# Optimization experiments

Measured on AMD Instinct MI355X. Metric: run time of the kernel, lower is better.

The kernel has to match this reference:

```python
import jax, jax.numpy as jnp
import numpy as np

N, E, F_IN, F_E, HID, HEADS = 20000, 320000, 256, 32, 128, 4
NEG_SLOPE = 0.2  # PyG GATConv default negative_slope


def _segment_softmax(logits, seg, num_segments):
    # logits: [E, H] softmax over edges sharing the same destination node
    m = jax.ops.segment_max(logits, seg, num_segments=num_segments)
    m = jnp.where(jnp.isfinite(m), m, 0.0)
    e = jnp.exp(logits - m[seg])
    s = jax.ops.segment_sum(e, seg, num_segments=num_segments)
    return e / s[seg]


def _gat_layer(x, edge_attr, src, dst, W, We, a_src, a_dst, a_edge, bias, num_nodes):
    H, C = a_src.shape
    h = (x @ W).reshape(-1, H, C)            # [N, H, C]
    he = (edge_attr @ We).reshape(-1, H, C)  # [E, H, C]
    alpha = (h * a_src).sum(-1)[src] + (h * a_dst).sum(-1)[dst] + (he * a_edge).sum(-1)
    alpha = jax.nn.leaky_relu(alpha, NEG_SLOPE)          # [E, H]
    alpha = _segment_softmax(alpha, dst, num_nodes)
    out = jax.ops.segment_sum(h[src] * alpha[..., None], dst, num_segments=num_nodes)
    return out.reshape(num_nodes, H * C) + bias


def setup_inputs() -> dict:
    key = jax.random.key(0)
    ks = jax.random.split(key, 20)
    s1 = 1.0 / np.sqrt(F_IN)
    s2 = 1.0 / np.sqrt(HID * HEADS)
    se = 1.0 / np.sqrt(F_E)
    sh = 1.0 / np.sqrt(HID)
    return {
        "x": jax.random.normal(ks[0], (N, F_IN), jnp.float32),
        "edge_index": jax.random.randint(ks[1], (2, E), 0, N),
        "edge_attr": jax.random.normal(ks[2], (E, F_E), jnp.float32),
        # GAT layer 1: in=F_IN, heads=HEADS, out=HID, concat=True
        "W1": jax.random.normal(ks[3], (F_IN, HEADS * HID), jnp.float32) * s1,
        "We1": jax.random.normal(ks[4], (F_E, HEADS * HID), jnp.float32) * se,
        "as1": jax.random.normal(ks[5], (HEADS, HID), jnp.float32) * sh,
        "ad1": jax.random.normal(ks[6], (HEADS, HID), jnp.float32) * sh,
        "ae1": jax.random.normal(ks[7], (HEADS, HID), jnp.float32) * sh,
        "b1": jnp.zeros((HEADS * HID,), jnp.float32),
        # GAT layer 2: in=HEADS*HID, heads=1, out=HID
        "W2": jax.random.normal(ks[8], (HEADS * HID, HID), jnp.float32) * s2,
        "We2": jax.random.normal(ks[9], (F_E, HID), jnp.float32) * se,
        "as2": jax.random.normal(ks[10], (1, HID), jnp.float32) * sh,
        "ad2": jax.random.normal(ks[11], (1, HID), jnp.float32) * sh,
        "ae2": jax.random.normal(ks[12], (1, HID), jnp.float32) * sh,
        "b2": jnp.zeros((HID,), jnp.float32),
        # projection head: Linear(HID,HID) -> PReLU -> Linear(HID,HID)
        "P1": jax.random.normal(ks[13], (HID, HID), jnp.float32) * sh,
        "pb1": jnp.zeros((HID,), jnp.float32),
        "prelu_a": jnp.float32(0.25),
        "P2": jax.random.normal(ks[14], (HID, HID), jnp.float32) * sh,
        "pb2": jnp.zeros((HID,), jnp.float32),
    }


def reference(x, edge_index, edge_attr, W1, We1, as1, ad1, ae1, b1,
              W2, We2, as2, ad2, ae2, b2, P1, pb1, prelu_a, P2, pb2):
    # eval mode: edge dropout / feature dropout are no-ops
    ei = jnp.concatenate([edge_index, edge_index[::-1]], axis=1)  # add reversed edges
    ea = jnp.concatenate([edge_attr, edge_attr], axis=0)
    src, dst = ei[0], ei[1]
    n = x.shape[0]
    h = jax.nn.elu(_gat_layer(x, ea, src, dst, W1, We1, as1, ad1, ae1, b1, n))
    h = jax.nn.elu(_gat_layer(h, ea, src, dst, W2, We2, as2, ad2, ae2, b2, n))
    z = h @ P1 + pb1
    z = jnp.where(z > 0, z, prelu_a * z)  # PReLU (single shared parameter)
    h_proj = z @ P2 + pb2
    g = jax.nn.sigmoid(h_proj.mean(axis=0))
    return h_proj, g
```

## Files before the change

kernel.cpp:

```cpp
#include <hip/hip_runtime.h>
#include <hip/hip_bf16.h>


#define NN    20000
#define EE    320000
#define E2    640000
#define FIN   256
#define FE    32
#define HIDD  128
#define NHEAD 4
#define HH    512

typedef unsigned short ushort_t;
typedef short frag8 __attribute__((ext_vector_type(8)));
typedef float f32x4 __attribute__((ext_vector_type(4)));

__device__ inline ushort_t f2bf(float f){
  unsigned x = __float_as_uint(f);
  unsigned r = (x + 0x7fffu + ((x>>16)&1u)) >> 16;
  return (ushort_t)r;
}
__device__ inline float bf2f(ushort_t u){ return __uint_as_float(((unsigned)u)<<16); }
__device__ inline float lo_of(unsigned v){ return __uint_as_float(v<<16); }
__device__ inline float hi_of(unsigned v){ return __uint_as_float(v & 0xffff0000u); }

__global__ void prep(const int* __restrict__ ei, int* __restrict__ cnt,
                     const float* __restrict__ x, ushort_t* __restrict__ xb,
                     const float* __restrict__ W1, ushort_t* __restrict__ W1t,
                     const float* __restrict__ W2, ushort_t* __restrict__ W2t,
                     const float* __restrict__ P1, ushort_t* __restrict__ P1th, ushort_t* __restrict__ P1tl,
                     const float* __restrict__ P2, ushort_t* __restrict__ P2th, ushort_t* __restrict__ P2tl,
                     const float* __restrict__ We1, const float* __restrict__ ae1,
                     const float* __restrict__ We2, const float* __restrict__ ae2,
                     float* __restrict__ v1, float* __restrict__ v2){
  int b = blockIdx.x, tid = threadIdx.x;
  if(b < 2500){
    int e = b*256 + tid;
    int dst = (e < EE) ? ei[EE + e] : ei[e - EE];
    atomicAdd(&cnt[dst], 1);
  } else if(b < 7500){
    int i = (b-2500)*256 + tid;
    float4 v = ((const float4*)x)[i];
    ushort4 o; o.x=f2bf(v.x); o.y=f2bf(v.y); o.z=f2bf(v.z); o.w=f2bf(v.w);
    ((ushort4*)xb)[i] = o;
  } else if(b < 8012){
    int idx = (b-7500)*256 + tid;
    int k = idx>>9, n = idx&511;
    W1t[n*FIN + k] = f2bf(W1[idx]);
  } else if(b < 8268){
    int idx = (b-8012)*256 + tid;
    int k = idx>>7, n = idx&127;
    W2t[n*HH + k] = f2bf(W2[idx]);
  } else if(b < 8332){
    int idx = (b-8268)*256 + tid;
    int k = idx>>7, n = idx&127;
    float v = P1[idx];
    ushort_t h = f2bf(v);
    P1th[n*HIDD + k] = h;
    P1tl[n*HIDD + k] = f2bf(v - bf2f(h));
  } else if(b < 8396){
    int idx = (b-8332)*256 + tid;
    int k = idx>>7, n = idx&127;
    float v = P2[idx];
    ushort_t h = f2bf(v);
    P2th[n*HIDD + k] = h;
    P2tl[n*HIDD + k] = f2bf(v - bf2f(h));
  } else {
    if(tid < FE*NHEAD){
      int f = tid>>2, h = tid&3;
      float s = 0.f;
      for(int c=0;c<HIDD;c++) s += We1[f*HH + h*HIDD + c] * ae1[h*HIDD + c];
      v1[f*4+h] = s;
    } else if(tid < FE*NHEAD + FE){
      int f = tid - FE*NHEAD;
      float s = 0.f;
      for(int c=0;c<HIDD;c++) s += We2[f*HIDD + c] * ae2[c];
      v2[f] = s;
    }
  }
}

__global__ void scan_k(const int* __restrict__ cnt, int* __restrict__ rowptr){
  __shared__ int sums[1024];
  int tid = threadIdx.x;
  const int per = (NN + 1023)/1024;
  int base = tid*per;
  int s = 0;
  for(int i=0;i<per;i++){ int idx=base+i; if(idx<NN) s += cnt[idx]; }
  sums[tid] = s; __syncthreads();
  for(int off=1; off<1024; off<<=1){
    int v = (tid>=off)? sums[tid-off] : 0;
    __syncthreads();
    sums[tid] += v;
    __syncthreads();
  }
  int run = (tid==0)? 0 : sums[tid-1];
  for(int i=0;i<per;i++){
    int idx = base+i;
    if(idx<=NN) rowptr[idx] = run;
    if(idx<NN)  run += cnt[idx];
  }
}

__global__ void csr_fill(const int* __restrict__ ei, const float* __restrict__ ea,
                         const float* __restrict__ v1, const float* __restrict__ v2,
                         const int* __restrict__ rowptr, int* __restrict__ fcnt,
                         int* __restrict__ csrc, float* __restrict__ cae1, float* __restrict__ cae2){
  __shared__ float sv1[FE*NHEAD];
  __shared__ float sv2[FE];
  int tid = threadIdx.x;
  if(tid < FE*NHEAD) sv1[tid] = v1[tid];
  if(tid < FE)       sv2[tid] = v2[tid];
  __syncthreads();
  int e = blockIdx.x*256 + tid;
  int a = ei[e], b = ei[EE+e];
  const float4* er4 = (const float4*)(ea + (long)e*FE);
  float a0=0,a1=0,a2=0,a3=0,ab=0;
  #pragma unroll
  for(int f4=0; f4<FE/4; f4++){
    float4 t = er4[f4];
    float tv[4] = {t.x, t.y, t.z, t.w};
    #pragma unroll
    for(int c=0;c<4;c++){
      int f = f4*4+c;
      float t1 = tv[c];
      a0 += t1*sv1[f*4+0]; a1 += t1*sv1[f*4+1]; a2 += t1*sv1[f*4+2]; a3 += t1*sv1[f*4+3];
      ab += t1*sv2[f];
    }
  }
  int pos = rowptr[b] + atomicAdd(&fcnt[b], 1);
  csrc[pos] = a;
  cae1[pos*4+0]=a0; cae1[pos*4+1]=a1; cae1[pos*4+2]=a2; cae1[pos*4+3]=a3;
  cae2[pos] = ab;
  pos = rowptr[a] + atomicAdd(&fcnt[a], 1);
  csrc[pos] = b;
  cae1[pos*4+0]=a0; cae1[pos*4+1]=a1; cae1[pos*4+2]=a2; cae1[pos*4+3]=a3;
  cae2[pos] = ab;
}

__global__ __launch_bounds__(256) void mfma_gemm(const ushort_t* __restrict__ A, const ushort_t* __restrict__ Bt,
                                                 ushort_t* __restrict__ C, int M, int N, int K){
  __shared__ ushort_t As[128*32];
  __shared__ ushort_t Bs[128*32];
  int tid = threadIdx.x;
  int m0 = blockIdx.y*128, n0 = blockIdx.x*128;
  int w = tid>>6, lane = tid&63;
  int qr = (w>>1)*64, qc = (w&1)*64;
  int lrow = lane&15, koff = (lane>>4)*8;
  f32x4 acc[4][4] = {};
  for(int k0=0; k0<K; k0+=32){
    #pragma unroll
    for(int rep=0;rep<2;rep++){
      int segid = tid + rep*256;
      int row = segid>>2, off = (segid&3)*8;
      int gr = m0 + row;
      int4 va = (gr<M) ? *(const int4*)(A + (long)gr*K + k0 + off) : int4{0,0,0,0};
      *(int4*)&As[row*32 + off] = va;
      int4 vb = *(const int4*)(Bt + (long)(n0+row)*K + k0 + off);
      *(int4*)&Bs[row*32 + off] = vb;
    }
    __syncthreads();
    frag8 af[4], bfr[4];
    #pragma unroll
    for(int i=0;i<4;i++) af[i]  = *(const frag8*)&As[(qr + i*16 + lrow)*32 + koff];
    #pragma unroll
    for(int j=0;j<4;j++) bfr[j] = *(const frag8*)&Bs[(qc + j*16 + lrow)*32 + koff];
    #pragma unroll
    for(int i=0;i<4;i++)
      #pragma unroll
      for(int j=0;j<4;j++)
        acc[i][j] = __builtin_amdgcn_mfma_f32_16x16x32_bf16(af[i], bfr[j], acc[i][j], 0,0,0);
    __syncthreads();
  }
  #pragma unroll
  for(int i=0;i<4;i++)
    #pragma unroll
    for(int j=0;j<4;j++)
      #pragma unroll
      for(int r=0;r<4;r++){
        int row = m0 + qr + i*16 + (lane>>4)*4 + r;
        int col = n0 + qc + j*16 + (lane&15);
        if(row<M) C[(long)row*N + col] = f2bf(acc[i][j][r]);
      }
}

__global__ __launch_bounds__(256) void mfma_gemm64(const ushort_t* __restrict__ A, const ushort_t* __restrict__ Bt,
                                                   ushort_t* __restrict__ C, int M, int N, int K){
  __shared__ ushort_t As[64*32];
  __shared__ ushort_t Bs[128*32];
  int tid = threadIdx.x;
  int m0 = blockIdx.y*64, n0 = blockIdx.x*128;
  int w = tid>>6, lane = tid&63;
  int qc = w*32;
  int lrow = lane&15, koff = (lane>>4)*8;
  f32x4 acc[4][2] = {};
  for(int k0=0; k0<K; k0+=32){
    {
      int row = tid>>2, off = (tid&3)*8;
      int gr = m0 + row;
      int4 va = (gr<M) ? *(const int4*)(A + (long)gr*K + k0 + off) : int4{0,0,0,0};
      *(int4*)&As[row*32 + off] = va;
    }
    #pragma unroll
    for(int rep=0;rep<2;rep++){
      int segid = tid + rep*256;
      int row = segid>>2, off = (segid&3)*8;
      int4 vb = *(const int4*)(Bt + (long)(n0+row)*K + k0 + off);
      *(int4*)&Bs[row*32 + off] = vb;
    }
    __syncthreads();
    frag8 af[4], bfr[2];
    #pragma unroll
    for(int i=0;i<4;i++) af[i]  = *(const frag8*)&As[(i*16 + lrow)*32 + koff];
    #pragma unroll
    for(int j=0;j<2;j++) bfr[j] = *(const frag8*)&Bs[(qc + j*16 + lrow)*32 + koff];
    #pragma unroll
    for(int i=0;i<4;i++)
      #pragma unroll
      for(int j=0;j<2;j++)
        acc[i][j] = __builtin_amdgcn_mfma_f32_16x16x32_bf16(af[i], bfr[j], acc[i][j], 0,0,0);
    __syncthreads();
  }
  #pragma unroll
  for(int i=0;i<4;i++)
    #pragma unroll
    for(int j=0;j<2;j++)
      #pragma unroll
      for(int r=0;r<4;r++){
        int row = m0 + i*16 + (lane>>4)*4 + r;
        int col = n0 + qc + j*16 + (lane&15);
        if(row<M) C[(long)row*N + col] = f2bf(acc[i][j][r]);
      }
}

__global__ __launch_bounds__(256) void mfma_proj(const float* __restrict__ A,
                                                 const ushort_t* __restrict__ Bth, const ushort_t* __restrict__ Btl,
                                                 float* __restrict__ C, int M,
                                                 const float* __restrict__ bias,
                                                 const float* __restrict__ prelu_a, int epi){
  __shared__ ushort_t Ash[64*32], Asl[64*32];
  __shared__ ushort_t Bsh[128*32], Bsl[128*32];
  int tid = threadIdx.x;
  int m0 = blockIdx.x*64;
  int w = tid>>6, lane = tid&63;
  int qc = w*32;
  int lrow = lane&15, koff2 = (lane>>4)*8;
  f32x4 acc[4][2] = {};
  for(int k0=0; k0<128; k0+=32){
    {
      int row = tid>>2, koff = (tid&3)*8;
      int gr = m0 + row;
      float4 u0{0,0,0,0}, u1{0,0,0,0};
      if(gr<M){
        u0 = *(const float4*)(A + (long)gr*HIDD + k0 + koff);
        u1 = *(const float4*)(A + (long)gr*HIDD + k0 + koff + 4);
      }
      float vv[8] = {u0.x,u0.y,u0.z,u0.w,u1.x,u1.y,u1.z,u1.w};
      unsigned ph[4], pl[4];
      #pragma unroll
      for(int c=0;c<4;c++){
        ushort_t h0 = f2bf(vv[2*c]),   l0 = f2bf(vv[2*c]   - bf2f(h0));
        ushort_t h1 = f2bf(vv[2*c+1]), l1 = f2bf(vv[2*c+1] - bf2f(h1));
        ph[c] = (unsigned)h0 | ((unsigned)h1<<16);
        pl[c] = (unsigned)l0 | ((unsigned)l1<<16);
      }
      *(uint4*)&Ash[row*32 + koff] = *(uint4*)ph;
      *(uint4*)&Asl[row*32 + koff] = *(uint4*)pl;
    }
    #pragma unroll
    for(int rep=0;rep<2;rep++){
      int segid = tid + rep*256;
      int row = segid>>2, off = (segid&3)*8;
      *(int4*)&Bsh[row*32 + off] = *(const int4*)(Bth + (long)row*HIDD + k0 + off);
      *(int4*)&Bsl[row*32 + off] = *(const int4*)(Btl + (long)row*HIDD + k0 + off);
    }
    __syncthreads();
    frag8 afh[4], afl[4], bfh[2], bfl[2];
    #pragma unroll
    for(int i=0;i<4;i++){
      afh[i] = *(const frag8*)&Ash[(i*16 + lrow)*32 + koff2];
      afl[i] = *(const frag8*)&Asl[(i*16 + lrow)*32 + koff2];
    }
    #pragma unroll
    for(int j=0;j<2;j++){
      bfh[j] = *(const frag8*)&Bsh[(qc + j*16 + lrow)*32 + koff2];
      bfl[j] = *(const frag8*)&Bsl[(qc + j*16 + lrow)*32 + koff2];
    }
    #pragma unroll
    for(int i=0;i<4;i++)
      #pragma unroll
      for(int j=0;j<2;j++){
        acc[i][j] = __builtin_amdgcn_mfma_f32_16x16x32_bf16(afh[i], bfh[j], acc[i][j], 0,0,0);
        acc[i][j] = __builtin_amdgcn_mfma_f32_16x16x32_bf16(afh[i], bfl[j], acc[i][j], 0,0,0);
        acc[i][j] = __builtin_amdgcn_mfma_f32_16x16x32_bf16(afl[i], bfh[j], acc[i][j], 0,0,0);
      }
    __syncthreads();
  }
  float ap = (epi==1)? prelu_a[0] : 0.f;
  #pragma unroll
  for(int i=0;i<4;i++)
    #pragma unroll
    for(int j=0;j<2;j++)
      #pragma unroll
      for(int r=0;r<4;r++){
        int row = m0 + i*16 + (lane>>4)*4 + r;
        int col = qc + j*16 + (lane&15);
        if(row<M){
          float v = acc[i][j][r] + bias[col];
          if(epi==1) v = v>0.f? v : ap*v;
          C[(long)row*HIDD + col] = v;
        }
      }
}


__global__ void node_attn1(const ushort_t* __restrict__ h1b, const float* __restrict__ as1,
                           const float* __restrict__ ad1, float* __restrict__ s1n, float* __restrict__ d1n){
  int n = blockIdx.x;
  int wv = threadIdx.x>>6, lane = threadIdx.x&63;
  unsigned v = *(const unsigned*)(h1b + (long)n*HH + wv*HIDD + 2*lane);
  float f0 = lo_of(v), f1 = hi_of(v);
  float s = f0*as1[wv*HIDD+2*lane] + f1*as1[wv*HIDD+2*lane+1];
  float d = f0*ad1[wv*HIDD+2*lane] + f1*ad1[wv*HIDD+2*lane+1];
  #pragma unroll
  for(int o=32;o>0;o>>=1){ s += __shfl_xor(s,o,64); d += __shfl_xor(d,o,64); }
  if(lane==0){ s1n[n*4+wv]=s; d1n[n*4+wv]=d; }
}

__global__ void node_attn2(const ushort_t* __restrict__ h2b, const float* __restrict__ as2,
                           const float* __restrict__ ad2, float* __restrict__ s2n, float* __restrict__ d2n){
  int n = blockIdx.x*4 + (threadIdx.x>>6);
  int lane = threadIdx.x&63;
  unsigned v = *(const unsigned*)(h2b + (long)n*HIDD + 2*lane);
  float f0 = lo_of(v), f1 = hi_of(v);
  float s = f0*as2[2*lane] + f1*as2[2*lane+1];
  float d = f0*ad2[2*lane] + f1*ad2[2*lane+1];
  #pragma unroll
  for(int o=32;o>0;o>>=1){ s += __shfl_xor(s,o,64); d += __shfl_xor(d,o,64); }
  if(lane==0){ s2n[n]=s; d2n[n]=d; }
}


__global__ void agg1(const ushort_t* __restrict__ h1b, const int* __restrict__ rowptr,
                     const int* __restrict__ csrc,
                     const float* __restrict__ s1n, const float* __restrict__ d1n,
                     const float* __restrict__ cae1, float* __restrict__ elog,
                     const float* __restrict__ b1, ushort_t* __restrict__ out1b){
  int n = blockIdx.x*4 + (threadIdx.x>>6);
  int lane = threadIdx.x&63;
  int beg = rowptr[n], end = rowptr[n+1];
  int h12 = lane&3;
  float dh = d1n[n*4 + h12];
  float m = -1e30f, ss = 0.f;
  for(int base=beg; base<end; base+=16){
    int e = base + (lane>>2);
    if(e<end){
      float t = s1n[csrc[e]*4 + h12] + dh + cae1[e*4 + h12];
      t = t>0.f? t : 0.2f*t;
      elog[e*4 + h12] = t;
      float nm = fmaxf(m, t);
      ss = ss*__expf(m-nm) + __expf(t-nm);
      m = nm;
    }
  }
  #pragma unroll
  for(int o=4;o<=32;o<<=1){
    float mo = __shfl_xor(m, o, 64), so = __shfl_xor(ss, o, 64);
    float nm = fmaxf(m, mo);
    ss = ss*__expf(m-nm) + so*__expf(mo-nm);
    m = nm;
  }
  float inv = ss>0.f ? 1.f/ss : 0.f;
  int hq = lane>>4;
  float mq   = __shfl(m,   hq, 64);
  float invq = __shfl(inv, hq, 64);
  float acc[8] = {};
  int i = beg;
  for(; i+3<end; i+=4){
    int s0 = csrc[i], s1 = csrc[i+1], s2 = csrc[i+2], s3 = csrc[i+3];
    float w0 = __expf(elog[i*4 + hq]     - mq)*invq;
    float w1 = __expf(elog[(i+1)*4 + hq] - mq)*invq;
    float w2 = __expf(elog[(i+2)*4 + hq] - mq)*invq;
    float w3 = __expf(elog[(i+3)*4 + hq] - mq)*invq;
    uint4 v0 = *(const uint4*)(h1b + (long)s0*HH + lane*8);
    uint4 v1 = *(const uint4*)(h1b + (long)s1*HH + lane*8);
    uint4 v2 = *(const uint4*)(h1b + (long)s2*HH + lane*8);
    uint4 v3 = *(const uint4*)(h1b + (long)s3*HH + lane*8);
    acc[0] += w0*lo_of(v0.x) + w1*lo_of(v1.x) + w2*lo_of(v2.x) + w3*lo_of(v3.x);
    acc[1] += w0*hi_of(v0.x) + w1*hi_of(v1.x) + w2*hi_of(v2.x) + w3*hi_of(v3.x);
    acc[2] += w0*lo_of(v0.y) + w1*lo_of(v1.y) + w2*lo_of(v2.y) + w3*lo_of(v3.y);
    acc[3] += w0*hi_of(v0.y) + w1*hi_of(v1.y) + w2*hi_of(v2.y) + w3*hi_of(v3.y);
    acc[4] += w0*lo_of(v0.z) + w1*lo_of(v1.z) + w2*lo_of(v2.z) + w3*lo_of(v3.z);
    acc[5] += w0*hi_of(v0.z) + w1*hi_of(v1.z) + w2*hi_of(v2.z) + w3*hi_of(v3.z);
    acc[6] += w0*lo_of(v0.w) + w1*lo_of(v1.w) + w2*lo_of(v2.w) + w3*lo_of(v3.w);
    acc[7] += w0*hi_of(v0.w) + w1*hi_of(v1.w) + w2*hi_of(v2.w) + w3*hi_of(v3.w);
  }
  for(; i<end; i++){
    int s0 = csrc[i];
    float w0 = __expf(elog[i*4 + hq] - mq)*invq;
    uint4 v0 = *(const uint4*)(h1b + (long)s0*HH + lane*8);
    acc[0] += w0*lo_of(v0.x); acc[1] += w0*hi_of(v0.x);
    acc[2] += w0*lo_of(v0.y); acc[3] += w0*hi_of(v0.y);
    acc[4] += w0*lo_of(v0.z); acc[5] += w0*hi_of(v0.z);
    acc[6] += w0*lo_of(v0.w); acc[7] += w0*hi_of(v0.w);
  }
  float4 bl = ((const float4*)b1)[lane*2];
  float4 bh = ((const float4*)b1)[lane*2+1];
  float bb[8] = {bl.x,bl.y,bl.z,bl.w,bh.x,bh.y,bh.z,bh.w};
  ushort_t o8[8];
  #pragma unroll
  for(int c=0;c<8;c++){
    float o = acc[c] + bb[c];
    o8[c] = f2bf(o>0.f? o : __expf(o)-1.f);
  }
  uint4 pk;
  pk.x = (unsigned)o8[0] | ((unsigned)o8[1]<<16);
  pk.y = (unsigned)o8[2] | ((unsigned)o8[3]<<16);
  pk.z = (unsigned)o8[4] | ((unsigned)o8[5]<<16);
  pk.w = (unsigned)o8[6] | ((unsigned)o8[7]<<16);
  *(uint4*)(out1b + (long)n*HH + lane*8) = pk;
}

__global__ void agg2(const ushort_t* __restrict__ h2b, const int* __restrict__ rowptr,
                     const int* __restrict__ csrc,
                     const float* __restrict__ s2n, const float* __restrict__ d2n,
                     const float* __restrict__ cae2, float* __restrict__ elog,
                     const float* __restrict__ b2, float* __restrict__ out2){
  int n = blockIdx.x*4 + (threadIdx.x>>6);
  int lane = threadIdx.x&63;
  int beg = rowptr[n], end = rowptr[n+1];
  float dn = d2n[n];
  float m = -1e30f, ss = 0.f;
  for(int e=beg+lane; e<end; e+=64){
    float t = s2n[csrc[e]] + dn + cae2[e];
    t = t>0.f? t : 0.2f*t;
    elog[e] = t;
    float nm = fmaxf(m, t);
    ss = ss*__expf(m-nm) + __expf(t-nm);
    m = nm;
  }
  #pragma unroll
  for(int o=1;o<=32;o<<=1){
    float mo = __shfl_xor(m, o, 64), so = __shfl_xor(ss, o, 64);
    float nm = fmaxf(m, mo);
    ss = ss*__expf(m-nm) + so*__expf(mo-nm);
    m = nm;
  }
  float inv = ss>0.f ? 1.f/ss : 0.f;
  float a0=0.f, a1=0.f;
  int i = beg;
  for(; i+3<end; i+=4){
    int s0 = csrc[i], s1 = csrc[i+1], s2 = csrc[i+2], s3 = csrc[i+3];
    float w0 = __expf(elog[i]-m)*inv;
    float w1 = __expf(elog[i+1]-m)*inv;
    float w2 = __expf(elog[i+2]-m)*inv;
    float w3 = __expf(elog[i+3]-m)*inv;
    unsigned v0 = *(const unsigned*)(h2b + (long)s0*HIDD + 2*lane);
    unsigned v1 = *(const unsigned*)(h2b + (long)s1*HIDD + 2*lane);
    unsigned v2 = *(const unsigned*)(h2b + (long)s2*HIDD + 2*lane);
    unsigned v3 = *(const unsigned*)(h2b + (long)s3*HIDD + 2*lane);
    a0 += w0*lo_of(v0) + w1*lo_of(v1) + w2*lo_of(v2) + w3*lo_of(v3);
    a1 += w0*hi_of(v0) + w1*hi_of(v1) + w2*hi_of(v2) + w3*hi_of(v3);
  }
  for(; i<end; i++){
    float w0 = __expf(elog[i]-m)*inv;
    unsigned v0 = *(const unsigned*)(h2b + (long)csrc[i]*HIDD + 2*lane);
    a0 += w0*lo_of(v0); a1 += w0*hi_of(v0);
  }
  float o0 = a0 + b2[2*lane];
  float o1 = a1 + b2[2*lane+1];
  float2 pk;
  pk.x = o0>0.f? o0 : __expf(o0)-1.f;
  pk.y = o1>0.f? o1 : __expf(o1)-1.f;
  *(float2*)(out2 + (long)n*HIDD + 2*lane) = pk;
}


__global__ void colsum(const float* __restrict__ hp, float* __restrict__ gbuf){
  int c = threadIdx.x;
  float acc = 0.f;
  for(int r = blockIdx.x; r < NN; r += gridDim.x) acc += hp[(long)r*HIDD + c];
  atomicAdd(&gbuf[c], acc);
}

__global__ void sigmoid_g(const float* __restrict__ gbuf, float* __restrict__ gout){
  int c = threadIdx.x;
  float m = gbuf[c] * (1.0f/NN);
  gout[c] = 1.f/(1.f+__expf(-m));
}


extern "C" void kernel_launch(void* const* d_in, const int* in_sizes, int n_in,
                              void* d_out, int out_size, void* d_ws, size_t ws_size,
                              hipStream_t stream){
  const float* x    = (const float*)d_in[0];
  const int*   ei   = (const int*)  d_in[1];
  const float* ea   = (const float*)d_in[2];
  const float* W1   = (const float*)d_in[3];
  const float* We1  = (const float*)d_in[4];
  const float* as1  = (const float*)d_in[5];
  const float* ad1  = (const float*)d_in[6];
  const float* ae1  = (const float*)d_in[7];
  const float* b1   = (const float*)d_in[8];
  const float* W2   = (const float*)d_in[9];
  const float* We2  = (const float*)d_in[10];
  const float* as2  = (const float*)d_in[11];
  const float* ad2  = (const float*)d_in[12];
  const float* ae2  = (const float*)d_in[13];
  const float* b2   = (const float*)d_in[14];
  const float* P1   = (const float*)d_in[15];
  const float* pb1  = (const float*)d_in[16];
  const float* pra  = (const float*)d_in[17];
  const float* P2   = (const float*)d_in[18];
  const float* pb2  = (const float*)d_in[19];
  float* out = (float*)d_out;

  char* wsp = (char*)d_ws;
  size_t off = 0;
  auto alloc = [&](size_t bytes)->char*{
    char* p = wsp + off;
    off += (bytes + 255) & ~(size_t)255;
    return p;
  };
  ushort_t* h1b  = (ushort_t*)alloc(sizeof(ushort_t)*(size_t)NN*HH);
  ushort_t* out1b= (ushort_t*)alloc(sizeof(ushort_t)*(size_t)NN*HH);
  ushort_t* h2b  = (ushort_t*)alloc(sizeof(ushort_t)*(size_t)NN*HIDD);
  float*    out2 = (float*)  alloc(sizeof(float)*(size_t)NN*HIDD);
  float*    zb   = (float*)  alloc(sizeof(float)*(size_t)NN*HIDD);
  ushort_t* xb   = (ushort_t*)alloc(sizeof(ushort_t)*(size_t)NN*FIN);
  ushort_t* W1t  = (ushort_t*)alloc(sizeof(ushort_t)*(size_t)HH*FIN);
  ushort_t* W2t  = (ushort_t*)alloc(sizeof(ushort_t)*(size_t)HIDD*HH);
  ushort_t* P1th = (ushort_t*)alloc(sizeof(ushort_t)*(size_t)HIDD*HIDD);
  ushort_t* P1tl = (ushort_t*)alloc(sizeof(ushort_t)*(size_t)HIDD*HIDD);
  ushort_t* P2th = (ushort_t*)alloc(sizeof(ushort_t)*(size_t)HIDD*HIDD);
  ushort_t* P2tl = (ushort_t*)alloc(sizeof(ushort_t)*(size_t)HIDD*HIDD);
  float* s1n   = (float*)alloc(sizeof(float)*NN*NHEAD);
  float* d1n   = (float*)alloc(sizeof(float)*NN*NHEAD);
  float* s2n   = (float*)alloc(sizeof(float)*NN);
  float* d2n   = (float*)alloc(sizeof(float)*NN);
  float* v1    = (float*)alloc(sizeof(float)*FE*NHEAD);
  float* v2    = (float*)alloc(sizeof(float)*FE);
  float* cae1  = (float*)alloc(sizeof(float)*(size_t)E2*NHEAD);
  float* elog1 = (float*)alloc(sizeof(float)*(size_t)E2*NHEAD);
  float* cae2  = (float*)alloc(sizeof(float)*(size_t)E2);
  float* elog2 = (float*)alloc(sizeof(float)*(size_t)E2);
  int*   rowptr= (int*)  alloc(sizeof(int)*(NN+1));
  int*   csrc  = (int*)  alloc(sizeof(int)*(size_t)E2);
  int*   cnt   = (int*)  alloc(sizeof(int)*NN);
  int*   fcnt  = (int*)  alloc(sizeof(int)*NN);
  float* gbuf  = (float*)alloc(sizeof(float)*HIDD);

  hipMemsetAsync(cnt, 0, 80128 + 80128 + 512, stream);

  prep    <<<8397, 256, 0, stream>>>(ei, cnt, x, xb, W1, W1t, W2, W2t,
                                     P1, P1th, P1tl, P2, P2th, P2tl,
                                     We1, ae1, We2, ae2, v1, v2);
  scan_k  <<<1, 1024, 0, stream>>>(cnt, rowptr);
  csr_fill<<<EE/256, 256, 0, stream>>>(ei, ea, v1, v2, rowptr, fcnt, csrc, cae1, cae2);

  mfma_gemm <<<dim3(HH/128, (NN+127)/128), 256, 0, stream>>>(xb, W1t, h1b, NN, HH, FIN);
  node_attn1<<<NN, 256, 0, stream>>>(h1b, as1, ad1, s1n, d1n);
  agg1      <<<NN/4, 256, 0, stream>>>(h1b, rowptr, csrc, s1n, d1n, cae1, elog1, b1, out1b);

  mfma_gemm64<<<dim3(1, (NN+63)/64), 256, 0, stream>>>(out1b, W2t, h2b, NN, HIDD, HH);
  node_attn2 <<<NN/4, 256, 0, stream>>>(h2b, as2, ad2, s2n, d2n);
  agg2       <<<NN/4, 256, 0, stream>>>(h2b, rowptr, csrc, s2n, d2n, cae2, elog2, b2, out2);

  mfma_proj<<<(NN+63)/64, 256, 0, stream>>>(out2, P1th, P1tl, zb, NN, pb1, pra, 1);
  mfma_proj<<<(NN+63)/64, 256, 0, stream>>>(zb,  P2th, P2tl, out, NN, pb2, nullptr, 0);

  colsum   <<<256, 128, 0, stream>>>(out, gbuf);
  sigmoid_g<<<1, 128, 0, stream>>>(gbuf, out + (size_t)NN*HIDD);
}
```

Baseline: 448.7 us.

## Fuse attention scores into GEMM epilogues, split agg1 edges, fuse column sum

New measurement: 432.7 us. 1.04x faster.

```diff
diff --git a/kernel.cpp b/kernel.cpp
--- a/kernel.cpp
+++ b/kernel.cpp
@@ -128,35 +128,40 @@
       ab += t1*sv2[f];
     }
   }
+  float4 c4; c4.x=a0; c4.y=a1; c4.z=a2; c4.w=a3;
   int pos = rowptr[b] + atomicAdd(&fcnt[b], 1);
   csrc[pos] = a;
-  cae1[pos*4+0]=a0; cae1[pos*4+1]=a1; cae1[pos*4+2]=a2; cae1[pos*4+3]=a3;
+  *(float4*)(cae1 + (size_t)pos*4) = c4;
   cae2[pos] = ab;
   pos = rowptr[a] + atomicAdd(&fcnt[a], 1);
   csrc[pos] = b;
-  cae1[pos*4+0]=a0; cae1[pos*4+1]=a1; cae1[pos*4+2]=a2; cae1[pos*4+3]=a3;
+  *(float4*)(cae1 + (size_t)pos*4) = c4;
   cae2[pos] = ab;
 }
 
-__global__ __launch_bounds__(256) void mfma_gemm(const ushort_t* __restrict__ A, const ushort_t* __restrict__ Bt,
-                                                 ushort_t* __restrict__ C, int M, int N, int K){
+__global__ __launch_bounds__(256) void gemm1_attn(const ushort_t* __restrict__ A, const ushort_t* __restrict__ Bt,
+                                                  ushort_t* __restrict__ C, int M,
+                                                  const float* __restrict__ as1, const float* __restrict__ ad1,
+                                                  float* __restrict__ s1n, float* __restrict__ d1n){
   __shared__ ushort_t As[128*32];
   __shared__ ushort_t Bs[128*32];
+  __shared__ float sred[2][128], dred[2][128];
   int tid = threadIdx.x;
-  int m0 = blockIdx.y*128, n0 = blockIdx.x*128;
+  int head = blockIdx.x;
+  int m0 = blockIdx.y*128, n0 = head*128;
   int w = tid>>6, lane = tid&63;
   int qr = (w>>1)*64, qc = (w&1)*64;
   int lrow = lane&15, koff = (lane>>4)*8;
   f32x4 acc[4][4] = {};
-  for(int k0=0; k0<K; k0+=32){
+  for(int k0=0; k0<FIN; k0+=32){
     #pragma unroll
     for(int rep=0;rep<2;rep++){
       int segid = tid + rep*256;
       int row = segid>>2, off = (segid&3)*8;
       int gr = m0 + row;
-      int4 va = (gr<M) ? *(const int4*)(A + (long)gr*K + k0 + off) : int4{0,0,0,0};
+      int4 va = (gr<M) ? *(const int4*)(A + (long)gr*FIN + k0 + off) : int4{0,0,0,0};
       *(int4*)&As[row*32 + off] = va;
-      int4 vb = *(const int4*)(Bt + (long)(n0+row)*K + k0 + off);
+      int4 vb = *(const int4*)(Bt + (long)(n0+row)*FIN + k0 + off);
       *(int4*)&Bs[row*32 + off] = vb;
     }
     __syncthreads();
@@ -180,32 +185,63 @@
       for(int r=0;r<4;r++){
         int row = m0 + qr + i*16 + (lane>>4)*4 + r;
         int col = n0 + qc + j*16 + (lane&15);
-        if(row<M) C[(long)row*N + col] = f2bf(acc[i][j][r]);
-      }
-}
-
-__global__ __launch_bounds__(256) void mfma_gemm64(const ushort_t* __restrict__ A, const ushort_t* __restrict__ Bt,
-                                                   ushort_t* __restrict__ C, int M, int N, int K){
+        if(row<M) C[(long)row*HH + col] = f2bf(acc[i][j][r]);
+      }
+  float a_s[4], a_d[4];
+  #pragma unroll
+  for(int j=0;j<4;j++){
+    a_s[j] = as1[head*HIDD + qc + j*16 + (lane&15)];
+    a_d[j] = ad1[head*HIDD + qc + j*16 + (lane&15)];
+  }
+  #pragma unroll
+  for(int i=0;i<4;i++)
+    #pragma unroll
+    for(int r=0;r<4;r++){
+      float sp = acc[i][0][r]*a_s[0] + acc[i][1][r]*a_s[1] + acc[i][2][r]*a_s[2] + acc[i][3][r]*a_s[3];
+      float dp = acc[i][0][r]*a_d[0] + acc[i][1][r]*a_d[1] + acc[i][2][r]*a_d[2] + acc[i][3][r]*a_d[3];
+      #pragma unroll
+      for(int o=1;o<=8;o<<=1){ sp += __shfl_xor(sp,o,64); dp += __shfl_xor(dp,o,64); }
+      if((lane&15)==0){
+        int rl = qr + i*16 + (lane>>4)*4 + r;
+        sred[w&1][rl] = sp;
+        dred[w&1][rl] = dp;
+      }
+    }
+  __syncthreads();
+  if(tid < 128){
+    int gr = m0 + tid;
+    if(gr < M){
+      s1n[gr*4 + head] = sred[0][tid] + sred[1][tid];
+      d1n[gr*4 + head] = dred[0][tid] + dred[1][tid];
+    }
+  }
+}
+
+__global__ __launch_bounds__(256) void gemm64_attn(const ushort_t* __restrict__ A, const ushort_t* __restrict__ Bt,
+                                                   ushort_t* __restrict__ C, int M,
+                                                   const float* __restrict__ as2, const float* __restrict__ ad2,
+                                                   float* __restrict__ s2n, float* __restrict__ d2n){
   __shared__ ushort_t As[64*32];
   __shared__ ushort_t Bs[128*32];
+  __shared__ float sred[4][64], dred[4][64];
   int tid = threadIdx.x;
-  int m0 = blockIdx.y*64, n0 = blockIdx.x*128;
+  int m0 = blockIdx.y*64;
   int w = tid>>6, lane = tid&63;
   int qc = w*32;
   int lrow = lane&15, koff = (lane>>4)*8;
   f32x4 acc[4][2] = {};
-  for(int k0=0; k0<K; k0+=32){
+  for(int k0=0; k0<HH; k0+=32){
     {
       int row = tid>>2, off = (tid&3)*8;
       int gr = m0 + row;
-      int4 va = (gr<M) ? *(const int4*)(A + (long)gr*K + k0 + off) : int4{0,0,0,0};
+      int4 va = (gr<M) ? *(const int4*)(A + (long)gr*HH + k0 + off) : int4{0,0,0,0};
       *(int4*)&As[row*32 + off] = va;
     }
     #pragma unroll
     for(int rep=0;rep<2;rep++){
       int segid = tid + rep*256;
       int row = segid>>2, off = (segid&3)*8;
-      int4 vb = *(const int4*)(Bt + (long)(n0+row)*K + k0 + off);
+      int4 vb = *(const int4*)(Bt + (long)row*HH + k0 + off);
       *(int4*)&Bs[row*32 + off] = vb;
     }
     __syncthreads();
@@ -228,16 +264,45 @@
       #pragma unroll
       for(int r=0;r<4;r++){
         int row = m0 + i*16 + (lane>>4)*4 + r;
-        int col = n0 + qc + j*16 + (lane&15);
-        if(row<M) C[(long)row*N + col] = f2bf(acc[i][j][r]);
-      }
+        int col = qc + j*16 + (lane&15);
+        if(row<M) C[(long)row*HIDD + col] = f2bf(acc[i][j][r]);
+      }
+  float a_s[2], a_d[2];
+  #pragma unroll
+  for(int j=0;j<2;j++){
+    a_s[j] = as2[qc + j*16 + (lane&15)];
+    a_d[j] = ad2[qc + j*16 + (lane&15)];
+  }
+  #pragma unroll
+  for(int i=0;i<4;i++)
+    #pragma unroll
+    for(int r=0;r<4;r++){
+      float sp = acc[i][0][r]*a_s[0] + acc[i][1][r]*a_s[1];
+      float dp = acc[i][0][r]*a_d[0] + acc[i][1][r]*a_d[1];
+      #pragma unroll
+      for(int o=1;o<=8;o<<=1){ sp += __shfl_xor(sp,o,64); dp += __shfl_xor(dp,o,64); }
+      if((lane&15)==0){
+        int rl = i*16 + (lane>>4)*4 + r;
+        sred[w][rl] = sp;
+        dred[w][rl] = dp;
+      }
+    }
+  __syncthreads();
+  if(tid < 64){
+    int gr = m0 + tid;
+    if(gr < M){
+      s2n[gr] = sred[0][tid]+sred[1][tid]+sred[2][tid]+sred[3][tid];
+      d2n[gr] = dred[0][tid]+dred[1][tid]+dred[2][tid]+dred[3][tid];
+    }
+  }
 }
 
 __global__ __launch_bounds__(256) void mfma_proj(const float* __restrict__ A,
                                                  const ushort_t* __restrict__ Bth, const ushort_t* __restrict__ Btl,
                                                  float* __restrict__ C, int M,
                                                  const float* __restrict__ bias,
-                                                 const float* __restrict__ prelu_a, int epi){
+                                                 const float* __restrict__ prelu_a, int epi,
+                                                 float* __restrict__ gbuf){
   __shared__ ushort_t Ash[64*32], Asl[64*32];
   __shared__ ushort_t Bsh[128*32], Bsl[128*32];
   int tid = threadIdx.x;
@@ -308,46 +373,37 @@
         if(row<M){
           float v = acc[i][j][r] + bias[col];
           if(epi==1) v = v>0.f? v : ap*v;
+          acc[i][j][r] = v;
           C[(long)row*HIDD + col] = v;
-        }
-      }
-}
-
-
-__global__ void node_attn1(const ushort_t* __restrict__ h1b, const float* __restrict__ as1,
-                           const float* __restrict__ ad1, float* __restrict__ s1n, float* __restrict__ d1n){
-  int n = blockIdx.x;
-  int wv = threadIdx.x>>6, lane = threadIdx.x&63;
-  unsigned v = *(const unsigned*)(h1b + (long)n*HH + wv*HIDD + 2*lane);
-  float f0 = lo_of(v), f1 = hi_of(v);
-  float s = f0*as1[wv*HIDD+2*lane] + f1*as1[wv*HIDD+2*lane+1];
-  float d = f0*ad1[wv*HIDD+2*lane] + f1*ad1[wv*HIDD+2*lane+1];
-  #pragma unroll
-  for(int o=32;o>0;o>>=1){ s += __shfl_xor(s,o,64); d += __shfl_xor(d,o,64); }
-  if(lane==0){ s1n[n*4+wv]=s; d1n[n*4+wv]=d; }
-}
-
-__global__ void node_attn2(const ushort_t* __restrict__ h2b, const float* __restrict__ as2,
-                           const float* __restrict__ ad2, float* __restrict__ s2n, float* __restrict__ d2n){
-  int n = blockIdx.x*4 + (threadIdx.x>>6);
-  int lane = threadIdx.x&63;
-  unsigned v = *(const unsigned*)(h2b + (long)n*HIDD + 2*lane);
-  float f0 = lo_of(v), f1 = hi_of(v);
-  float s = f0*as2[2*lane] + f1*as2[2*lane+1];
-  float d = f0*ad2[2*lane] + f1*ad2[2*lane+1];
-  #pragma unroll
-  for(int o=32;o>0;o>>=1){ s += __shfl_xor(s,o,64); d += __shfl_xor(d,o,64); }
-  if(lane==0){ s2n[n]=s; d2n[n]=d; }
-}
-
-
-__global__ void agg1(const ushort_t* __restrict__ h1b, const int* __restrict__ rowptr,
+        } else acc[i][j][r] = 0.f;
+      }
+  if(epi==0){
+    #pragma unroll
+    for(int j=0;j<2;j++){
+      float cp = 0.f;
+      #pragma unroll
+      for(int i=0;i<4;i++)
+        #pragma unroll
+        for(int r=0;r<4;r++) cp += acc[i][j][r];
+      cp += __shfl_xor(cp,16,64);
+      cp += __shfl_xor(cp,32,64);
+      if((lane>>4)==0) atomicAdd(&gbuf[qc + j*16 + (lane&15)], cp);
+    }
+  }
+}
+
+
+__global__ __launch_bounds__(512) void agg1(const ushort_t* __restrict__ h1b, const int* __restrict__ rowptr,
                      const int* __restrict__ csrc,
                      const float* __restrict__ s1n, const float* __restrict__ d1n,
                      const float* __restrict__ cae1, float* __restrict__ elog,
                      const float* __restrict__ b1, ushort_t* __restrict__ out1b){
-  int n = blockIdx.x*4 + (threadIdx.x>>6);
-  int lane = threadIdx.x&63;
+  __shared__ float part[4][512];
+  int tid = threadIdx.x;
+  int nodeLoc = tid>>7;
+  int wv = (tid>>6)&1;
+  int lane = tid&63;
+  int n = blockIdx.x*4 + nodeLoc;
   int beg = rowptr[n], end = rowptr[n+1];
   int h12 = lane&3;
   float dh = d1n[n*4 + h12];
@@ -357,7 +413,7 @@
     if(e<end){
       float t = s1n[csrc[e]*4 + h12] + dh + cae1[e*4 + h12];
       t = t>0.f? t : 0.2f*t;
-      elog[e*4 + h12] = t;
+      if(wv==0) elog[e*4 + h12] = t;
       float nm = fmaxf(m, t);
       ss = ss*__expf(m-nm) + __expf(t-nm);
       m = nm;
@@ -374,9 +430,14 @@
   int hq = lane>>4;
   float mq   = __shfl(m,   hq, 64);
   float invq = __shfl(inv, hq, 64);
+  __syncthreads();
+  int deg = end-beg;
+  int half = (deg+1)>>1;
+  int gb = beg + wv*half;
+  int ge = wv ? end : beg+half;
   float acc[8] = {};
-  int i = beg;
-  for(; i+3<end; i+=4){
+  int i = gb;
+  for(; i+3<ge; i+=4){
     int s0 = csrc[i], s1 = csrc[i+1], s2 = csrc[i+2], s3 = csrc[i+3];
     float w0 = __expf(elog[i*4 + hq]     - mq)*invq;
     float w1 = __expf(elog[(i+1)*4 + hq] - mq)*invq;
@@ -395,7 +456,7 @@
     acc[6] += w0*lo_of(v0.w) + w1*lo_of(v1.w) + w2*lo_of(v2.w) + w3*lo_of(v3.w);
     acc[7] += w0*hi_of(v0.w) + w1*hi_of(v1.w) + w2*hi_of(v2.w) + w3*hi_of(v3.w);
   }
-  for(; i<end; i++){
+  for(; i<ge; i++){
     int s0 = csrc[i];
     float w0 = __expf(elog[i*4 + hq] - mq)*invq;
     uint4 v0 = *(const uint4*)(h1b + (long)s0*HH + lane*8);
@@ -404,21 +465,30 @@
     acc[4] += w0*lo_of(v0.z); acc[5] += w0*hi_of(v0.z);
     acc[6] += w0*lo_of(v0.w); acc[7] += w0*hi_of(v0.w);
   }
-  float4 bl = ((const float4*)b1)[lane*2];
-  float4 bh = ((const float4*)b1)[lane*2+1];
-  float bb[8] = {bl.x,bl.y,bl.z,bl.w,bh.x,bh.y,bh.z,bh.w};
-  ushort_t o8[8];
-  #pragma unroll
-  for(int c=0;c<8;c++){
-    float o = acc[c] + bb[c];
-    o8[c] = f2bf(o>0.f? o : __expf(o)-1.f);
-  }
-  uint4 pk;
-  pk.x = (unsigned)o8[0] | ((unsigned)o8[1]<<16);
-  pk.y = (unsigned)o8[2] | ((unsigned)o8[3]<<16);
-  pk.z = (unsigned)o8[4] | ((unsigned)o8[5]<<16);
-  pk.w = (unsigned)o8[6] | ((unsigned)o8[7]<<16);
-  *(uint4*)(out1b + (long)n*HH + lane*8) = pk;
+  if(wv==1){
+    #pragma unroll
+    for(int c=0;c<8;c++) part[nodeLoc][c*64 + lane] = acc[c];
+  }
+  __syncthreads();
+  if(wv==0){
+    #pragma unroll
+    for(int c=0;c<8;c++) acc[c] += part[nodeLoc][c*64 + lane];
+    float4 bl = ((const float4*)b1)[lane*2];
+    float4 bh = ((const float4*)b1)[lane*2+1];
+    float bb[8] = {bl.x,bl.y,bl.z,bl.w,bh.x,bh.y,bh.z,bh.w};
+    ushort_t o8[8];
+    #pragma unroll
+    for(int c=0;c<8;c++){
+      float o = acc[c] + bb[c];
+      o8[c] = f2bf(o>0.f? o : __expf(o)-1.f);
+    }
+    uint4 pk;
+    pk.x = (unsigned)o8[0] | ((unsigned)o8[1]<<16);
+    pk.y = (unsigned)o8[2] | ((unsigned)o8[3]<<16);
+    pk.z = (unsigned)o8[4] | ((unsigned)o8[5]<<16);
+    pk.w = (unsigned)o8[6] | ((unsigned)o8[7]<<16);
+    *(uint4*)(out1b + (long)n*HH + lane*8) = pk;
+  }
 }
 
 __global__ void agg2(const ushort_t* __restrict__ h2b, const int* __restrict__ rowptr,
@@ -473,14 +543,6 @@
   pk.x = o0>0.f? o0 : __expf(o0)-1.f;
   pk.y = o1>0.f? o1 : __expf(o1)-1.f;
   *(float2*)(out2 + (long)n*HIDD + 2*lane) = pk;
-}
-
-
-__global__ void colsum(const float* __restrict__ hp, float* __restrict__ gbuf){
-  int c = threadIdx.x;
-  float acc = 0.f;
-  for(int r = blockIdx.x; r < NN; r += gridDim.x) acc += hp[(long)r*HIDD + c];
-  atomicAdd(&gbuf[c], acc);
 }
 
 __global__ void sigmoid_g(const float* __restrict__ gbuf, float* __restrict__ gout){
@@ -558,17 +620,14 @@
   scan_k  <<<1, 1024, 0, stream>>>(cnt, rowptr);
   csr_fill<<<EE/256, 256, 0, stream>>>(ei, ea, v1, v2, rowptr, fcnt, csrc, cae1, cae2);
 
-  mfma_gemm <<<dim3(HH/128, (NN+127)/128), 256, 0, stream>>>(xb, W1t, h1b, NN, HH, FIN);
-  node_attn1<<<NN, 256, 0, stream>>>(h1b, as1, ad1, s1n, d1n);
-  agg1      <<<NN/4, 256, 0, stream>>>(h1b, rowptr, csrc, s1n, d1n, cae1, elog1, b1, out1b);
-
-  mfma_gemm64<<<dim3(1, (NN+63)/64), 256, 0, stream>>>(out1b, W2t, h2b, NN, HIDD, HH);
-  node_attn2 <<<NN/4, 256, 0, stream>>>(h2b, as2, ad2, s2n, d2n);
+  gemm1_attn<<<dim3(NHEAD, (NN+127)/128), 256, 0, stream>>>(xb, W1t, h1b, NN, as1, ad1, s1n, d1n);
+  agg1      <<<NN/4, 512, 0, stream>>>(h1b, rowptr, csrc, s1n, d1n, cae1, elog1, b1, out1b);
+
+  gemm64_attn<<<dim3(1, (NN+63)/64), 256, 0, stream>>>(out1b, W2t, h2b, NN, as2, ad2, s2n, d2n);
   agg2       <<<NN/4, 256, 0, stream>>>(h2b, rowptr, csrc, s2n, d2n, cae2, elog2, b2, out2);
 
-  mfma_proj<<<(NN+63)/64, 256, 0, stream>>>(out2, P1th, P1tl, zb, NN, pb1, pra, 1);
-  mfma_proj<<<(NN+63)/64, 256, 0, stream>>>(zb,  P2th, P2tl, out, NN, pb2, nullptr, 0);
-
-  colsum   <<<256, 128, 0, stream>>>(out, gbuf);
+  mfma_proj<<<(NN+63)/64, 256, 0, stream>>>(out2, P1th, P1tl, zb, NN, pb1, pra, 1, nullptr);
+  mfma_proj<<<(NN+63)/64, 256, 0, stream>>>(zb,  P2th, P2tl, out, NN, pb2, nullptr, 0, gbuf);
+
   sigmoid_g<<<1, 128, 0, stream>>>(gbuf, out + (size_t)NN*HIDD);
 }
```
